# Performance work log

Measured on AMD Instinct MI355X. Metric: run time of the kernel, lower is better.

The kernel has to match this reference:

```python
import jax, jax.numpy as jnp
import numpy as np

C = 256; Ca = C // 2; WH = 8; WW = 8; K = 3; NH = 8; HD = Ca // NH
EPS_LN = 1e-5; EPS_BN = 1e-5

def _rel_pos_idx(wh, ww):
    coords = np.stack(np.meshgrid(np.arange(wh), np.arange(ww), indexing='ij'))  # (2,wh,ww)
    flat = coords.reshape(2, -1)
    rel = (flat[:, :, None] - flat[:, None, :]).transpose(1, 2, 0).astype(np.int64)  # (N,N,2)
    rel[..., 0] += wh - 1
    rel[..., 1] += ww - 1
    rel[..., 0] *= 2 * ww - 1
    return jnp.asarray(rel.sum(-1))  # (N,N)

REL_IDX = _rel_pos_idx(WH, WW)

def _ln(x, g, b):
    m = x.mean(-1, keepdims=True)
    v = x.var(-1, keepdims=True)
    return (x - m) / jnp.sqrt(v + EPS_LN) * g + b

def _bn(x, g, b):  # eval-mode BN, running_mean=0, running_var=1; x is NCHW
    return x * (g / np.sqrt(1.0 + EPS_BN))[None, :, None, None] + b[None, :, None, None]

def _conv1x1(x, w, b):  # w: (O, I)
    return jnp.einsum('bchw,oc->bohw', x, w) + b[None, :, None, None]

def _rwp(x, h, w, wh, ww):  # windows (B*nW, wh*ww, c) -> image (B, c, h, w)
    Bn, N, c = x.shape
    nh, nw = h // wh, w // ww
    B = Bn // (nh * nw)
    x = x.reshape(B, nh, nw, wh, ww, c)
    return x.transpose(0, 5, 1, 3, 2, 4).reshape(B, c, h, w)

def _wp(x, wh, ww):  # image (B, c, h, w) -> windows (B*nW, wh*ww, c)
    B, c, h, w = x.shape
    x = x.reshape(B, c, h // wh, wh, w // ww, ww)
    return x.transpose(0, 2, 4, 3, 5, 1).reshape(-1, wh * ww, c)

def _gelu(t):
    return jax.nn.gelu(t, approximate=False)

def forward(x, rel_pos_bias, attn_w, attn_b, attn_ln_g, attn_ln_b,
            conv_w, conv_b, conv_bn_g, conv_bn_b,
            ci_w1, ci_b1, ci_bn_g, ci_bn_b, ci_w2, ci_b2,
            pr_w, pr_b, cn_bn_g, cn_bn_b,
            qkv_w, qkv_b,
            si_w1, si_b1, si_bn_g, si_bn_b, si_w2, si_b2,
            an_g, an_b, out_w, out_b, h, w):
    B_, N, Cfull = x.shape
    x_attn = _ln(x @ attn_w + attn_b, attn_ln_g, attn_ln_b)  # (B_, N, Ca)
    # conv branch -- note: source applies RWP to raw x (proj_cnn output is dead code)
    x_img = _rwp(x, h, w, WH, WW)  # (B, C, h, w)
    pad = K // 2
    x_cnn = jax.lax.conv_general_dilated(
        x_img, conv_w, (1, 1), [(pad, pad), (pad, pad)],
        dimension_numbers=('NCHW', 'OIHW', 'NCHW'), feature_group_count=Cfull)
    x_cnn = _gelu(_bn(x_cnn + conv_b[None, :, None, None], conv_bn_g, conv_bn_b))
    gap = x_cnn.mean((2, 3), keepdims=True)  # (B, C, 1, 1)
    ci = _conv1x1(gap, ci_w1, ci_b1)
    ci = _gelu(_bn(ci, ci_bn_g, ci_bn_b))
    ci = _conv1x1(ci, ci_w2, ci_b2)  # (B, Ca, 1, 1)
    x_cnn = _conv1x1(x_cnn, pr_w, pr_b)  # (B, Ca, h, w)
    # windowed attention
    qkv = (x_attn @ qkv_w + qkv_b).reshape(B_, N, 3, NH, HD).transpose(2, 0, 3, 1, 4)
    q, k, v = qkv[0], qkv[1], qkv[2]  # each (B_, NH, N, HD)
    B = ci.shape[0]
    ci_s = jax.nn.sigmoid(ci).reshape(B, 1, NH, 1, HD)
    v = (v.reshape(B, B_ // B, NH, N, HD) * ci_s).reshape(B_, NH, N, HD)
    scale = HD ** -0.5
    attn = jnp.einsum('bhnd,bhmd->bhnm', q * scale, k)
    bias = rel_pos_bias[REL_IDX]  # (N, N, NH)
    attn = jax.nn.softmax(attn + bias.transpose(2, 0, 1)[None], axis=-1)
    x_attn = jnp.einsum('bhnm,bhmd->bhnd', attn, v).transpose(0, 2, 1, 3).reshape(B_, N, Ca)
    # spatial interaction gating of conv branch
    x_sp = _rwp(x_attn, h, w, WH, WW)  # (B, Ca, h, w)
    si = _conv1x1(x_sp, si_w1, si_b1)
    si = _gelu(_bn(si, si_bn_g, si_bn_b))
    si = _conv1x1(si, si_w2, si_b2)  # (B, 1, h, w)
    x_cnn = jax.nn.sigmoid(si * x_cnn)
    x_cnn = _bn(x_cnn, cn_bn_g, cn_bn_b)
    x_cnn = _wp(x_cnn, WH, WW)  # (B_, N, Ca)
    x_attn = _ln(x_attn, an_g, an_b)
    return jnp.concatenate([x_attn, x_cnn], axis=-1) @ out_w + out_b

def setup_inputs() -> dict:
    key = jax.random.key(0)
    ks = jax.random.split(key, 12)
    B_, N = 2048, WH * WW
    s = 0.02
    return dict(
        x=jax.random.normal(ks[0], (B_, N, C), jnp.float32),
        rel_pos_bias=jax.random.uniform(ks[1], ((2 * WH - 1) * (2 * WW - 1), NH), jnp.float32),
        attn_w=jax.random.normal(ks[2], (C, Ca)) * s, attn_b=jnp.zeros((Ca,)),
        attn_ln_g=jnp.ones((Ca,)), attn_ln_b=jnp.zeros((Ca,)),
        conv_w=jax.random.normal(ks[3], (C, 1, K, K)) * s, conv_b=jnp.zeros((C,)),
        conv_bn_g=jnp.ones((C,)), conv_bn_b=jnp.zeros((C,)),
        ci_w1=jax.random.normal(ks[4], (C // 8, C)) * s, ci_b1=jnp.zeros((C // 8,)),
        ci_bn_g=jnp.ones((C // 8,)), ci_bn_b=jnp.zeros((C // 8,)),
        ci_w2=jax.random.normal(ks[5], (Ca, C // 8)) * s, ci_b2=jnp.zeros((Ca,)),
        pr_w=jax.random.normal(ks[6], (Ca, C)) * s, pr_b=jnp.zeros((Ca,)),
        cn_bn_g=jnp.ones((Ca,)), cn_bn_b=jnp.zeros((Ca,)),
        qkv_w=jax.random.normal(ks[7], (Ca, 3 * Ca)) * s, qkv_b=jnp.zeros((3 * Ca,)),
        si_w1=jax.random.normal(ks[8], (C // 16, Ca)) * s, si_b1=jnp.zeros((C // 16,)),
        si_bn_g=jnp.ones((C // 16,)), si_bn_b=jnp.zeros((C // 16,)),
        si_w2=jax.random.normal(ks[9], (1, C // 16)) * s, si_b2=jnp.zeros((1,)),
        an_g=jnp.ones((Ca,)), an_b=jnp.zeros((Ca,)),
        out_w=jax.random.normal(ks[10], (C, C)) * s, out_b=jnp.zeros((C,)),
        h=64, w=64,
    )

def reference(x, rel_pos_bias, attn_w, attn_b, attn_ln_g, attn_ln_b,
              conv_w, conv_b, conv_bn_g, conv_bn_b,
              ci_w1, ci_b1, ci_bn_g, ci_bn_b, ci_w2, ci_b2,
              pr_w, pr_b, cn_bn_g, cn_bn_b,
              qkv_w, qkv_b,
              si_w1, si_b1, si_bn_g, si_bn_b, si_w2, si_b2,
              an_g, an_b, out_w, out_b, h, w):
    return forward(x, rel_pos_bias, attn_w, attn_b, attn_ln_g, attn_ln_b,
                   conv_w, conv_b, conv_bn_g, conv_bn_b,
                   ci_w1, ci_b1, ci_bn_g, ci_bn_b, ci_w2, ci_b2,
                   pr_w, pr_b, cn_bn_g, cn_bn_b,
                   qkv_w, qkv_b,
                   si_w1, si_b1, si_bn_g, si_bn_b, si_w2, si_b2,
                   an_g, an_b, out_w, out_b, h, w)
```

## Files before the change

### kernel.cpp

```cpp
#include <hip/hip_runtime.h>
#include <math.h>


#define BNR 0.9999950000374998f

typedef __attribute__((ext_vector_type(8))) short short8;
typedef __attribute__((ext_vector_type(4))) float f32x4;
typedef __attribute__((ext_vector_type(4))) _Float16 half4;
typedef __attribute__((ext_vector_type(8))) _Float16 half8;
typedef __attribute__((ext_vector_type(2))) _Float16 h2v;

__device__ __forceinline__ float gelu_f(float x) {
  const float z = x * (1.0f + 0.044715f * x * x);
  return x / (1.0f + __expf(-1.5957691216057308f * z));
}
__device__ __forceinline__ unsigned short f2bf(float f) {
  unsigned int u = __builtin_bit_cast(unsigned int, f);
  u += 0x7fffu + ((u >> 16) & 1u);
  return (unsigned short)(u >> 16);
}
__device__ __forceinline__ float bf2f(unsigned short h) {
  unsigned int u = ((unsigned int)h) << 16;
  return __builtin_bit_cast(float, u);
}
__device__ __forceinline__ void ld8(const unsigned short* p, float* o) {
  const short8 v = *(const short8*)p;
#pragma unroll
  for (int i = 0; i < 8; ++i) o[i] = bf2f((unsigned short)v[i]);
}
__device__ __forceinline__ unsigned int pkh(float a, float b) {
  return __builtin_bit_cast(unsigned int, __builtin_amdgcn_cvt_pkrtz(a, b));
}

#define ATI(r, ch) (((r) << 8) + ((((ch) ^ ((r)&7))) << 3))

__global__ __launch_bounds__(256) void kpack(
    const float* __restrict__ aw, const float* __restrict__ qw,
    const float* __restrict__ prw, const float* __restrict__ ow,
    const float* __restrict__ sw1, unsigned short* __restrict__ awp,
    unsigned short* __restrict__ qwp, unsigned short* __restrict__ prwp,
    unsigned short* __restrict__ owp, unsigned short* __restrict__ sw1p) {
  const int b = blockIdx.x;
  const float* src; unsigned short* dst; int fs, K, N, NT, trans, f16o;
  if (b < 64)       { fs = b;       src = aw;  dst = awp;  K = 256; N = 128; NT = 8;  trans = 0; f16o = 0; }
  else if (b < 160) { fs = b - 64;  src = qw;  dst = qwp;  K = 128; N = 384; NT = 24; trans = 0; f16o = 0; }
  else if (b < 224) { fs = b - 160; src = prw; dst = prwp; K = 256; N = 128; NT = 8;  trans = 1; f16o = 1; }
  else if (b < 352) { fs = b - 224; src = ow;  dst = owp;  K = 256; N = 256; NT = 16; trans = 0; f16o = 0; }
  else              { fs = b - 352; src = sw1; dst = sw1p; K = 128; N = 16;  NT = 1;  trans = 1; f16o = 0; }
  const int ks = fs / NT, nt = fs % NT;
  for (int idx = threadIdx.x; idx < 512; idx += 256) {
    const int l = idx >> 3, i = idx & 7;
    const int k = ks * 32 + ((l >> 4) << 3) + i, n = nt * 16 + (l & 15);
    const float v = trans ? src[n * K + k] : src[k * N + n];
    dst[(fs * 64 + l) * 8 + i] =
        f16o ? __builtin_bit_cast(unsigned short, (_Float16)v) : f2bf(v);
  }
}

__global__ __launch_bounds__(256) void kbias(const float* __restrict__ rpb,
                                             unsigned short* __restrict__ bt) {
  const int i = blockIdx.x * 256 + threadIdx.x;
  const int h = i >> 12, n = (i >> 6) & 63, m = i & 63;
  const int ny = n >> 3, nx = n & 7, my = m >> 3, mx = m & 7;
  const float v = rpb[((ny - my + 7) * 15 + (nx - mx + 7)) * 8 + h];
  bt[i] = __builtin_bit_cast(unsigned short, (_Float16)v);
}

__global__ __launch_bounds__(256) void k1_attn_ln(
    const float* __restrict__ x, const unsigned short* __restrict__ awp,
    const float* __restrict__ ab, const float* __restrict__ lg,
    const float* __restrict__ lb, unsigned short* __restrict__ xattn,
    unsigned short* __restrict__ xb) {
  const int tid = threadIdx.x, w = tid >> 6, l = tid & 63;
  const int lr = l & 15, lg4 = l >> 4;
  const int r0 = blockIdx.x * 64 + w * 16;
  const float* xp = x + (size_t)(r0 + lr) * 256 + lg4 * 8;
  unsigned short* xbp = xb + (size_t)(r0 + lr) * 256 + lg4 * 8;
  short8 a[8];
#pragma unroll
  for (int ks = 0; ks < 8; ++ks) {
    const float4 f0 = *(const float4*)(xp + ks * 32);
    const float4 f1 = *(const float4*)(xp + ks * 32 + 4);
    short8 av;
    av[0] = f2bf(f0.x); av[1] = f2bf(f0.y); av[2] = f2bf(f0.z); av[3] = f2bf(f0.w);
    av[4] = f2bf(f1.x); av[5] = f2bf(f1.y); av[6] = f2bf(f1.z); av[7] = f2bf(f1.w);
    a[ks] = av;
    uint4 hv;
    hv.x = pkh(f0.x, f0.y); hv.y = pkh(f0.z, f0.w);
    hv.z = pkh(f1.x, f1.y); hv.w = pkh(f1.z, f1.w);
    *(uint4*)(xbp + ks * 32) = hv;
  }
  f32x4 acc[8];
#pragma unroll
  for (int nt = 0; nt < 8; ++nt) acc[nt] = (f32x4)0.f;
#pragma unroll
  for (int nt = 0; nt < 8; ++nt)
#pragma unroll
    for (int ks = 0; ks < 8; ++ks) {
      const short8 bfr = *(const short8*)(awp + ((ks * 8 + nt) * 64 + l) * 8);
      acc[nt] = __builtin_amdgcn_mfma_f32_16x16x32_bf16(a[ks], bfr, acc[nt], 0, 0, 0);
    }
  float bias[8], gam[8], bet[8];
#pragma unroll
  for (int nt = 0; nt < 8; ++nt) {
    const int col = nt * 16 + lr;
    bias[nt] = ab[col]; gam[nt] = lg[col]; bet[nt] = lb[col];
  }
#pragma unroll
  for (int j = 0; j < 4; ++j) {
    float s = 0.f, qq = 0.f;
#pragma unroll
    for (int nt = 0; nt < 8; ++nt) {
      const float v = acc[nt][j] + bias[nt];
      acc[nt][j] = v; s += v; qq += v * v;
    }
    s += __shfl_xor(s, 1); s += __shfl_xor(s, 2);
    s += __shfl_xor(s, 4); s += __shfl_xor(s, 8);
    qq += __shfl_xor(qq, 1); qq += __shfl_xor(qq, 2);
    qq += __shfl_xor(qq, 4); qq += __shfl_xor(qq, 8);
    const float mean = s * (1.f / 128.f);
    const float var = qq * (1.f / 128.f) - mean * mean;
    const float rstd = rsqrtf(var + 1e-5f);
    const int row = r0 + lg4 * 4 + j;
#pragma unroll
    for (int nt = 0; nt < 8; ++nt)
      xattn[(size_t)row * 128 + nt * 16 + lr] =
          f2bf((acc[nt][j] - mean) * rstd * gam[nt] + bet[nt]);
  }
}

__global__ __launch_bounds__(256) void k25_conv(
    const unsigned short* __restrict__ xb, const float* __restrict__ cw,
    const float* __restrict__ cb, const float* __restrict__ bg,
    const float* __restrict__ bb, const unsigned short* __restrict__ prwp,
    const float* __restrict__ prb, unsigned short* __restrict__ xpr,
    float* __restrict__ gpart) {
  __shared__ unsigned short gl[32][264];
  const int tid = threadIdx.x;
  const int bid = (blockIdx.x & 7) * 512 + (blockIdx.x >> 3);
  const int b = bid >> 7;
  const int y = (bid >> 1) & 63;
  const int xt = (bid & 1) * 32;
  const int w = tid >> 6, l = tid & 63;
  {
    const int c0 = l << 2;
    h2v w01[9], w23[9];
#pragma unroll
    for (int k = 0; k < 9; ++k) {
      w01[k][0] = (_Float16)cw[(c0 + 0) * 9 + k];
      w01[k][1] = (_Float16)cw[(c0 + 1) * 9 + k];
      w23[k][0] = (_Float16)cw[(c0 + 2) * 9 + k];
      w23[k][1] = (_Float16)cw[(c0 + 3) * 9 + k];
    }
    const float4 cbf = *(const float4*)&cb[c0];
    float4 scf = *(const float4*)&bg[c0];
    scf.x *= BNR; scf.y *= BNR; scf.z *= BNR; scf.w *= BNR;
    const float4 sbf = *(const float4*)&bb[c0];
    h2v cb01 = {(_Float16)cbf.x, (_Float16)cbf.y};
    h2v cb23 = {(_Float16)cbf.z, (_Float16)cbf.w};
    h2v sc01 = {(_Float16)scf.x, (_Float16)scf.y};
    h2v sc23 = {(_Float16)scf.z, (_Float16)scf.w};
    h2v sb01 = {(_Float16)sbf.x, (_Float16)sbf.y};
    h2v sb23 = {(_Float16)sbf.z, (_Float16)sbf.w};
    float4 gsum = make_float4(0.f, 0.f, 0.f, 0.f);
    const int px0 = xt + w * 8;
#pragma unroll
    for (int sc2 = 0; sc2 < 2; ++sc2) {
      const int p0 = px0 + sc2 * 4;
      h2v v0[3][6], v1[3][6];
#pragma unroll
      for (int dy = 0; dy < 3; ++dy) {
        const int yy = y + dy - 1;
        const bool vy = (unsigned)yy < 64u;
        const int ybase = vy ? ((b * 64 + (yy >> 3) * 8) * 64 + (yy & 7) * 8) : 0;
#pragma unroll
        for (int q = 0; q < 6; ++q) {
          const int xx = p0 - 1 + q;
          h2v a = (h2v)(_Float16)0.f, c = (h2v)(_Float16)0.f;
          if (vy && (unsigned)xx < 64u) {
            const int row = ybase + (xx >> 3) * 64 + (xx & 7);
            const uint2 u = *(const uint2*)&xb[(size_t)row * 256 + c0];
            a = __builtin_bit_cast(h2v, u.x);
            c = __builtin_bit_cast(h2v, u.y);
          }
          v0[dy][q] = a; v1[dy][q] = c;
        }
      }
#pragma unroll
      for (int p = 0; p < 4; ++p) {
        h2v s0 = cb01, s1 = cb23;
#pragma unroll
        for (int dy = 0; dy < 3; ++dy)
#pragma unroll
          for (int dx = 0; dx < 3; ++dx) {
            s0 = w01[dy * 3 + dx] * v0[dy][p + dx] + s0;
            s1 = w23[dy * 3 + dx] * v1[dy][p + dx] + s1;
          }
        s0 = s0 * sc01 + sb01;
        s1 = s1 * sc23 + sb23;
        const float g0 = gelu_f((float)s0[0]), g1 = gelu_f((float)s0[1]);
        const float g2 = gelu_f((float)s1[0]), g3 = gelu_f((float)s1[1]);
        uint2 pk;
        pk.x = pkh(g0, g1); pk.y = pkh(g2, g3);
        *(uint2*)&gl[w * 8 + sc2 * 4 + p][c0] = pk;
        gsum.x += g0; gsum.y += g1; gsum.z += g2; gsum.w += g3;
      }
    }
    *(float4*)&gpart[(size_t)bid * 256 + c0] = gsum;
  }
  __syncthreads();
  const int lr = l & 15, lg4 = l >> 4;
  const int mr0 = (w & 1) * 16, nt0 = (w >> 1) * 4;
  half8 a[8];
#pragma unroll
  for (int ks = 0; ks < 8; ++ks)
    a[ks] = __builtin_bit_cast(half8,
                               *(const short8*)&gl[mr0 + lr][ks * 32 + lg4 * 8]);
  f32x4 acc[4];
#pragma unroll
  for (int nt = 0; nt < 4; ++nt) acc[nt] = (f32x4)0.f;
#pragma unroll
  for (int nt = 0; nt < 4; ++nt)
#pragma unroll
    for (int ks = 0; ks < 8; ++ks) {
      const half8 bfr = __builtin_bit_cast(
          half8, *(const short8*)(prwp + ((ks * 8 + nt0 + nt) * 64 + l) * 8));
      acc[nt] = __builtin_amdgcn_mfma_f32_16x16x32_f16(a[ks], bfr, acc[nt], 0, 0, 0);
    }
#pragma unroll
  for (int nt = 0; nt < 4; ++nt) {
    const int col = (nt0 + nt) * 16 + lr;
    const float bv = prb[col];
#pragma unroll
    for (int j = 0; j < 4; ++j) {
      const int pix = (b * 64 + y) * 64 + xt + mr0 + lg4 * 4 + j;
      xpr[(size_t)pix * 128 + col] = f2bf(acc[nt][j] + bv);
    }
  }
}

__global__ __launch_bounds__(128) void k3_ci(
    const float* __restrict__ gp, const float* __restrict__ w1,
    const float* __restrict__ b1, const float* __restrict__ g1,
    const float* __restrict__ bb1, const float* __restrict__ w2,
    const float* __restrict__ b2, float* __restrict__ cis) {
  __shared__ float gm[256];
  __shared__ float c1[32];
  const int b = blockIdx.x, tid = threadIdx.x;
  for (int c = tid; c < 256; c += 128) {
    float s = 0.f;
    for (int p = 0; p < 128; ++p) s += gp[(size_t)(b * 128 + p) * 256 + c];
    gm[c] = s * (1.f / 4096.f);
  }
  __syncthreads();
  if (tid < 32) {
    float s = b1[tid];
    for (int c = 0; c < 256; ++c) s = fmaf(gm[c], w1[tid * 256 + c], s);
    s = s * (g1[tid] * BNR) + bb1[tid];
    c1[tid] = gelu_f(s);
  }
  __syncthreads();
  float s = b2[tid];
#pragma unroll
  for (int i = 0; i < 32; ++i) s = fmaf(c1[i], w2[tid * 32 + i], s);
  cis[b * 128 + tid] = 1.f / (1.f + __expf(-s));
}

__global__ __launch_bounds__(256) void k4_attn(
    const unsigned short* __restrict__ xa, const unsigned short* __restrict__ qwp,
    const float* __restrict__ qb, const float* __restrict__ cis,
    const unsigned short* __restrict__ biasT, unsigned short* __restrict__ attn) {
  __shared__ _Float16 Qs[64][130];
  __shared__ _Float16 Ks[64][130];
  __shared__ _Float16 VT[128][66];
  __shared__ float cisl[128];
  __shared__ float qbl[384];
  const int tid = threadIdx.x;
  const int win = blockIdx.x, img = win >> 6;
  for (int i = tid; i < 128; i += 256) cisl[i] = cis[img * 128 + i];
  for (int i = tid; i < 384; i += 256) qbl[i] = qb[i];
  const int w = tid >> 6, l = tid & 63, lr = l & 15, lg4 = l >> 4;
  short8 a[4];
  const unsigned short* ap = xa + (size_t)(win * 64 + w * 16 + lr) * 128 + lg4 * 8;
#pragma unroll
  for (int ks = 0; ks < 4; ++ks) a[ks] = *(const short8*)(ap + ks * 32);
  f32x4 acc[24];
#pragma unroll
  for (int nt = 0; nt < 24; ++nt) acc[nt] = (f32x4)0.f;
#pragma unroll
  for (int nt = 0; nt < 24; ++nt)
#pragma unroll
    for (int ks = 0; ks < 4; ++ks) {
      const short8 bfr = *(const short8*)(qwp + ((ks * 24 + nt) * 64 + l) * 8);
      acc[nt] = __builtin_amdgcn_mfma_f32_16x16x32_bf16(a[ks], bfr, acc[nt], 0, 0, 0);
    }
  __syncthreads();
#pragma unroll
  for (int nt = 0; nt < 24; ++nt) {
    const int col = nt * 16 + lr;
#pragma unroll
    for (int j = 0; j < 4; ++j) {
      const int row = w * 16 + lg4 * 4 + j;
      const float v = acc[nt][j] + qbl[col];
      if (nt < 8) Qs[row][col] = (_Float16)(v * 0.25f);
      else if (nt < 16) Ks[row][col - 128] = (_Float16)v;
      else VT[col - 256][row] = (_Float16)(v * cisl[col - 256]);
    }
  }
  __syncthreads();
  for (int hi = 0; hi < 2; ++hi) {
    const int h = w * 2 + hi;
    half4 aK[4], bQ[4], bV[4];
#pragma unroll
    for (int mt = 0; mt < 4; ++mt)
      aK[mt] = *(const half4*)&Ks[mt * 16 + lr][h * 16 + lg4 * 4];
#pragma unroll
    for (int nt = 0; nt < 4; ++nt)
      bQ[nt] = *(const half4*)&Qs[nt * 16 + lr][h * 16 + lg4 * 4];
#pragma unroll
    for (int kt = 0; kt < 4; ++kt)
      bV[kt] = *(const half4*)&VT[h * 16 + lr][kt * 16 + lg4 * 4];
    f32x4 s[4][4];
#pragma unroll
    for (int mt = 0; mt < 4; ++mt)
#pragma unroll
      for (int nt = 0; nt < 4; ++nt)
        s[mt][nt] = __builtin_amdgcn_mfma_f32_16x16x16f16(aK[mt], bQ[nt],
                                                          (f32x4)0.f, 0, 0, 0);
#pragma unroll
    for (int nt = 0; nt < 4; ++nt) {
      const int n = nt * 16 + lr;
      const unsigned short* bp = biasT + (((h << 6) + n) << 6);
#pragma unroll
      for (int mt = 0; mt < 4; ++mt) {
        const half4 b4 = *(const half4*)(bp + mt * 16 + lg4 * 4);
        s[mt][nt][0] += (float)b4[0];
        s[mt][nt][1] += (float)b4[1];
        s[mt][nt][2] += (float)b4[2];
        s[mt][nt][3] += (float)b4[3];
      }
    }
    float inv[4];
#pragma unroll
    for (int nt = 0; nt < 4; ++nt) {
      float m0 = -1e30f;
#pragma unroll
      for (int mt = 0; mt < 4; ++mt)
#pragma unroll
        for (int r = 0; r < 4; ++r) m0 = fmaxf(m0, s[mt][nt][r]);
      m0 = fmaxf(m0, __shfl_xor(m0, 16));
      m0 = fmaxf(m0, __shfl_xor(m0, 32));
      float d0 = 0.f;
#pragma unroll
      for (int mt = 0; mt < 4; ++mt)
#pragma unroll
        for (int r = 0; r < 4; ++r) {
          const float e = __expf(s[mt][nt][r] - m0);
          s[mt][nt][r] = e;
          d0 += e;
        }
      d0 += __shfl_xor(d0, 16);
      d0 += __shfl_xor(d0, 32);
      inv[nt] = 1.f / d0;
    }
    half4 pa[4][4];
#pragma unroll
    for (int nt = 0; nt < 4; ++nt)
#pragma unroll
      for (int kt = 0; kt < 4; ++kt) {
        half4 p;
#pragma unroll
        for (int r = 0; r < 4; ++r) p[r] = (_Float16)(s[kt][nt][r] * inv[nt]);
        pa[nt][kt] = p;
      }
    f32x4 o[4];
#pragma unroll
    for (int nt = 0; nt < 4; ++nt) o[nt] = (f32x4)0.f;
#pragma unroll
    for (int nt = 0; nt < 4; ++nt)
#pragma unroll
      for (int kt = 0; kt < 4; ++kt)
        o[nt] = __builtin_amdgcn_mfma_f32_16x16x16f16(pa[nt][kt], bV[kt], o[nt], 0, 0, 0);
#pragma unroll
    for (int nt = 0; nt < 4; ++nt)
#pragma unroll
      for (int r = 0; r < 4; ++r) {
        const int token = win * 64 + nt * 16 + lg4 * 4 + r;
        attn[(size_t)token * 128 + h * 16 + lr] = f2bf(o[nt][r]);
      }
  }
}

__global__ __launch_bounds__(256) void k6_tail(
    const unsigned short* __restrict__ attn, const unsigned short* __restrict__ xpr,
    const unsigned short* __restrict__ sw1p, const float* __restrict__ sb1,
    const float* __restrict__ sgc, const float* __restrict__ sbc,
    const float* __restrict__ sw2, const float* __restrict__ sb2,
    const float* __restrict__ cg, const float* __restrict__ cbb,
    const float* __restrict__ ag, const float* __restrict__ abb,
    const unsigned short* __restrict__ owp, const float* __restrict__ ob,
    float* __restrict__ out) {
  __shared__ unsigned short At[64 * 256];
  __shared__ float sifl[64];
  __shared__ float statl[64][2];
  const int tid = threadIdx.x;
  const int R0 = blockIdx.x * 64;
  const int w = tid >> 6, l = tid & 63, lr = l & 15, lg4 = l >> 4;
  for (int i = tid; i < 1024; i += 256) {
    const int r = i >> 4, c16 = i & 15;
    *(uint4*)&At[ATI(r, c16)] =
        *(const uint4*)&attn[(size_t)(R0 + r) * 128 + c16 * 8];
    const int R = R0 + r, win = R >> 6, tt = R & 63;
    const int bimg = win >> 6, wy = (win >> 3) & 7, wx = win & 7;
    const int pix = (bimg * 64 + wy * 8 + (tt >> 3)) * 64 + wx * 8 + (tt & 7);
    *(uint4*)&At[ATI(r, 16 + c16)] =
        *(const uint4*)&xpr[(size_t)pix * 128 + c16 * 8];
  }
  __syncthreads();
  {
    const int r = tid >> 2, q = tid & 3;
    float xv[32];
#pragma unroll
    for (int b8 = 0; b8 < 4; ++b8) ld8(&At[ATI(r, q * 4 + b8)], xv + b8 * 8);
    float ps = 0.f, pq = 0.f;
#pragma unroll
    for (int j = 0; j < 32; ++j) { ps += xv[j]; pq += xv[j] * xv[j]; }
    ps += __shfl_xor(ps, 1); ps += __shfl_xor(ps, 2);
    pq += __shfl_xor(pq, 1); pq += __shfl_xor(pq, 2);
    if (q == 0) {
      const float mean = ps * (1.f / 128.f);
      const float var = pq * (1.f / 128.f) - mean * mean;
      statl[r][0] = mean;
      statl[r][1] = rsqrtf(var + 1e-5f);
    }
  }
  {
    const int row = w * 16 + lr;
    f32x4 sa = (f32x4)0.f;
#pragma unroll
    for (int ks = 0; ks < 4; ++ks) {
      const short8 a4 = *(const short8*)&At[ATI(row, ks * 4 + lg4)];
      const short8 bfr = *(const short8*)(sw1p + (ks * 64 + l) * 8);
      sa = __builtin_amdgcn_mfma_f32_16x16x32_bf16(a4, bfr, sa, 0, 0, 0);
    }
    const float sb1v = sb1[lr], g1v = sgc[lr] * BNR, b1v = sbc[lr];
    const float w2v = sw2[lr], sb2v = sb2[0];
#pragma unroll
    for (int j = 0; j < 4; ++j) {
      float s = (sa[j] + sb1v) * g1v + b1v;
      float p = gelu_f(s) * w2v;
      p += __shfl_xor(p, 1); p += __shfl_xor(p, 2);
      p += __shfl_xor(p, 4); p += __shfl_xor(p, 8);
      if (lr == 0) sifl[w * 16 + lg4 * 4 + j] = p + sb2v;
    }
  }
  __syncthreads();
  {
    const int c = tid & 127;
    const float agv = ag[c], abbv = abb[c];
    const float cgv = cg[c] * BNR, cbbv = cbb[c];
#pragma unroll
    for (int k = 0; k < 32; ++k) {
      const int r = (tid >> 7) + k * 2;
      const int ia = ATI(r, c >> 3) + (c & 7);
      const int ic = ATI(r, 16 + (c >> 3)) + (c & 7);
      float a = bf2f(At[ia]);
      a = (a - statl[r][0]) * statl[r][1] * agv + abbv;
      At[ia] = f2bf(a);
      const float cv = bf2f(At[ic]);
      const float g = 1.f / (1.f + __expf(-sifl[r] * cv));
      At[ic] = f2bf(g * cgv + cbbv);
    }
  }
  __syncthreads();
  const int row = w * 16 + lr;
  short8 a[8];
#pragma unroll
  for (int ks = 0; ks < 8; ++ks)
    a[ks] = *(const short8*)&At[ATI(row, ks * 4 + lg4)];
  f32x4 acc[16];
#pragma unroll
  for (int nt = 0; nt < 16; ++nt) acc[nt] = (f32x4)0.f;
#pragma unroll
  for (int nt = 0; nt < 16; ++nt)
#pragma unroll
    for (int ks = 0; ks < 8; ++ks) {
      const short8 bfr = *(const short8*)(owp + ((ks * 16 + nt) * 64 + l) * 8);
      acc[nt] = __builtin_amdgcn_mfma_f32_16x16x32_bf16(a[ks], bfr, acc[nt], 0, 0, 0);
    }
#pragma unroll
  for (int nt = 0; nt < 16; ++nt) {
    const int col = nt * 16 + lr;
    const float bv = ob[col];
#pragma unroll
    for (int j = 0; j < 4; ++j)
      out[(size_t)(R0 + w * 16 + lg4 * 4 + j) * 256 + col] = acc[nt][j] + bv;
  }
}

extern "C" void kernel_launch(void* const* d_in, const int* in_sizes, int n_in,
                              void* d_out, int out_size, void* d_ws,
                              size_t ws_size, hipStream_t stream) {
  (void)in_sizes; (void)n_in; (void)out_size; (void)ws_size;
  const float* x      = (const float*)d_in[0];
  const float* rpb    = (const float*)d_in[1];
  const float* attn_w = (const float*)d_in[2];
  const float* attn_b = (const float*)d_in[3];
  const float* aln_g  = (const float*)d_in[4];
  const float* aln_b  = (const float*)d_in[5];
  const float* conv_w = (const float*)d_in[6];
  const float* conv_b = (const float*)d_in[7];
  const float* cbn_g  = (const float*)d_in[8];
  const float* cbn_b  = (const float*)d_in[9];
  const float* ci_w1  = (const float*)d_in[10];
  const float* ci_b1  = (const float*)d_in[11];
  const float* ci_bg  = (const float*)d_in[12];
  const float* ci_bb  = (const float*)d_in[13];
  const float* ci_w2  = (const float*)d_in[14];
  const float* ci_b2  = (const float*)d_in[15];
  const float* pr_w   = (const float*)d_in[16];
  const float* pr_b   = (const float*)d_in[17];
  const float* cn_g   = (const float*)d_in[18];
  const float* cn_b   = (const float*)d_in[19];
  const float* qkv_w  = (const float*)d_in[20];
  const float* qkv_b  = (const float*)d_in[21];
  const float* si_w1  = (const float*)d_in[22];
  const float* si_b1  = (const float*)d_in[23];
  const float* si_bg  = (const float*)d_in[24];
  const float* si_bb  = (const float*)d_in[25];
  const float* si_w2  = (const float*)d_in[26];
  const float* si_b2  = (const float*)d_in[27];
  const float* an_g   = (const float*)d_in[28];
  const float* an_b   = (const float*)d_in[29];
  const float* out_w  = (const float*)d_in[30];
  const float* out_b  = (const float*)d_in[31];

  unsigned short* xb    = (unsigned short*)d_ws;
  unsigned short* xattn = xb + 33554432;
  unsigned short* attn  = xattn + 16777216;
  unsigned short* xpr   = attn + 16777216;
  float* gpart = (float*)(xpr + 16777216);
  float* cis   = gpart + 1048576;
  unsigned short* awp   = (unsigned short*)(cis + 4096);
  unsigned short* qwp   = awp + 32768;
  unsigned short* prwp  = qwp + 49152;
  unsigned short* owp   = prwp + 32768;
  unsigned short* sw1p  = owp + 65536;
  unsigned short* biasT = sw1p + 2048;

  kpack<<<356, 256, 0, stream>>>(attn_w, qkv_w, pr_w, out_w, si_w1,
                                 awp, qwp, prwp, owp, sw1p);
  kbias<<<128, 256, 0, stream>>>(rpb, biasT);
  k1_attn_ln<<<2048, 256, 0, stream>>>(x, awp, attn_b, aln_g, aln_b, xattn, xb);
  k25_conv<<<4096, 256, 0, stream>>>(xb, conv_w, conv_b, cbn_g, cbn_b, prwp,
                                     pr_b, xpr, gpart);
  k3_ci<<<32, 128, 0, stream>>>(gpart, ci_w1, ci_b1, ci_bg, ci_bb, ci_w2,
                                ci_b2, cis);
  k4_attn<<<2048, 256, 0, stream>>>(xattn, qwp, qkv_b, cis, biasT, attn);
  k6_tail<<<2048, 256, 0, stream>>>(attn, xpr, sw1p, si_b1, si_bg, si_bb,
                                    si_w2, si_b2, cn_g, cn_b, an_g, an_b,
                                    owp, out_b, (float*)d_out);
}
```

Before: 305.0 us.

## Repartition QKV projection per head-pair warp to drop block-wide syncs

The QKV projection in the attention kernel is re-tiled so each wavefront computes Q, K and V for its own two heads across all 64 rows, instead of 16 rows across all 384 outputs. Each wave then writes into a private shared-memory slice and reads it back only itself, which removes both __syncthreads barriers and the shared staging of bias and channel-scale vectors. In exchange, every wave now loads all 64 rows of the input (more redundant global/L1 reads of xa), while weight fragments are reused across four row tiles.

```diff
diff --git a/kernel.cpp b/kernel.cpp
--- a/kernel.cpp
+++ b/kernel.cpp
@@ -270,56 +270,69 @@
     const unsigned short* __restrict__ xa, const unsigned short* __restrict__ qwp,
     const float* __restrict__ qb, const float* __restrict__ cis,
     const unsigned short* __restrict__ biasT, unsigned short* __restrict__ attn) {
-  __shared__ _Float16 Qs[64][130];
-  __shared__ _Float16 Ks[64][130];
-  __shared__ _Float16 VT[128][66];
-  __shared__ float cisl[128];
-  __shared__ float qbl[384];
+  __shared__ _Float16 QS[4][64][36];
+  __shared__ _Float16 KS[4][64][36];
+  __shared__ _Float16 VTS[4][32][68];
   const int tid = threadIdx.x;
   const int win = blockIdx.x, img = win >> 6;
-  for (int i = tid; i < 128; i += 256) cisl[i] = cis[img * 128 + i];
-  for (int i = tid; i < 384; i += 256) qbl[i] = qb[i];
   const int w = tid >> 6, l = tid & 63, lr = l & 15, lg4 = l >> 4;
-  short8 a[4];
-  const unsigned short* ap = xa + (size_t)(win * 64 + w * 16 + lr) * 128 + lg4 * 8;
-#pragma unroll
-  for (int ks = 0; ks < 4; ++ks) a[ks] = *(const short8*)(ap + ks * 32);
-  f32x4 acc[24];
-#pragma unroll
-  for (int nt = 0; nt < 24; ++nt) acc[nt] = (f32x4)0.f;
-#pragma unroll
-  for (int nt = 0; nt < 24; ++nt)
-#pragma unroll
-    for (int ks = 0; ks < 4; ++ks) {
-      const short8 bfr = *(const short8*)(qwp + ((ks * 24 + nt) * 64 + l) * 8);
-      acc[nt] = __builtin_amdgcn_mfma_f32_16x16x32_bf16(a[ks], bfr, acc[nt], 0, 0, 0);
-    }
-  __syncthreads();
-#pragma unroll
-  for (int nt = 0; nt < 24; ++nt) {
-    const int col = nt * 16 + lr;
-#pragma unroll
-    for (int j = 0; j < 4; ++j) {
-      const int row = w * 16 + lg4 * 4 + j;
-      const float v = acc[nt][j] + qbl[col];
-      if (nt < 8) Qs[row][col] = (_Float16)(v * 0.25f);
-      else if (nt < 16) Ks[row][col - 128] = (_Float16)v;
-      else VT[col - 256][row] = (_Float16)(v * cisl[col - 256]);
-    }
-  }
-  __syncthreads();
+  int ntg6[6];
+#pragma unroll
+  for (int nt6 = 0; nt6 < 6; ++nt6)
+    ntg6[nt6] = (nt6 < 2) ? 2 * w + nt6 : (nt6 < 4) ? 6 + 2 * w + nt6
+                                                    : 12 + 2 * w + nt6;
+  float qbv[6];
+#pragma unroll
+  for (int nt6 = 0; nt6 < 6; ++nt6) qbv[nt6] = qb[ntg6[nt6] * 16 + lr];
+  float cisv[2];
+#pragma unroll
+  for (int t = 0; t < 2; ++t) cisv[t] = cis[img * 128 + w * 32 + t * 16 + lr];
+  f32x4 acc[4][6];
+#pragma unroll
+  for (int mt = 0; mt < 4; ++mt)
+#pragma unroll
+    for (int nt6 = 0; nt6 < 6; ++nt6) acc[mt][nt6] = (f32x4)0.f;
+#pragma unroll
+  for (int ks = 0; ks < 4; ++ks) {
+    short8 a[4];
+#pragma unroll
+    for (int mt = 0; mt < 4; ++mt)
+      a[mt] = *(const short8*)(xa + (size_t)(win * 64 + mt * 16 + lr) * 128 +
+                               ks * 32 + lg4 * 8);
+#pragma unroll
+    for (int nt6 = 0; nt6 < 6; ++nt6) {
+      const short8 bfr =
+          *(const short8*)(qwp + ((ks * 24 + ntg6[nt6]) * 64 + l) * 8);
+#pragma unroll
+      for (int mt = 0; mt < 4; ++mt)
+        acc[mt][nt6] = __builtin_amdgcn_mfma_f32_16x16x32_bf16(a[mt], bfr,
+                                                               acc[mt][nt6], 0, 0, 0);
+    }
+  }
+#pragma unroll
+  for (int mt = 0; mt < 4; ++mt)
+#pragma unroll
+    for (int nt6 = 0; nt6 < 6; ++nt6)
+#pragma unroll
+      for (int j = 0; j < 4; ++j) {
+        const int row = mt * 16 + lg4 * 4 + j;
+        const float v = acc[mt][nt6][j] + qbv[nt6];
+        if (nt6 < 2) QS[w][row][nt6 * 16 + lr] = (_Float16)(v * 0.25f);
+        else if (nt6 < 4) KS[w][row][(nt6 - 2) * 16 + lr] = (_Float16)v;
+        else VTS[w][(nt6 - 4) * 16 + lr][row] = (_Float16)(v * cisv[nt6 - 4]);
+      }
   for (int hi = 0; hi < 2; ++hi) {
     const int h = w * 2 + hi;
     half4 aK[4], bQ[4], bV[4];
 #pragma unroll
     for (int mt = 0; mt < 4; ++mt)
-      aK[mt] = *(const half4*)&Ks[mt * 16 + lr][h * 16 + lg4 * 4];
+      aK[mt] = *(const half4*)&KS[w][mt * 16 + lr][hi * 16 + lg4 * 4];
 #pragma unroll
     for (int nt = 0; nt < 4; ++nt)
-      bQ[nt] = *(const half4*)&Qs[nt * 16 + lr][h * 16 + lg4 * 4];
+      bQ[nt] = *(const half4*)&QS[w][nt * 16 + lr][hi * 16 + lg4 * 4];
 #pragma unroll
     for (int kt = 0; kt < 4; ++kt)
-      bV[kt] = *(const half4*)&VT[h * 16 + lr][kt * 16 + lg4 * 4];
+      bV[kt] = *(const half4*)&VTS[w][hi * 16 + lr][kt * 16 + lg4 * 4];
     f32x4 s[4][4];
 #pragma unroll
     for (int mt = 0; mt < 4; ++mt)
```

New measurement: 313.6 us. +2.8%, slower.
